# Performance work log

Measured on AMD Instinct MI355X. Metric: run time of the kernel, lower is better.

The kernel has to match this reference:

```python
import jax, jax.numpy as jnp
import numpy as np

IN_FEATURES = 4096
OUT_FEATURES = 4096
DENSE_OUT = int(0.85 * OUT_FEATURES)          # 3481
SPARSE_OUT = OUT_FEATURES - DENSE_OUT         # 615


def setup_inputs() -> dict:
    key = jax.random.key(0)
    kx, kw = jax.random.split(key)
    x = jax.random.normal(kx, (4, 2048, IN_FEATURES), dtype=jnp.float32)
    weights = jax.random.normal(kw, (OUT_FEATURES, IN_FEATURES), dtype=jnp.float32)
    return {"x": x, "weights": weights}


def reference(x, weights):
    # Module partitions weight rows: first SPARSE_OUT rows go through sputnik
    # SpMM, the remaining DENSE_OUT rows through a cutlass GEMM, then outputs
    # are concatenated as [sparse, dense] -> identical to x @ weights.T.
    size_out = x.shape[:-1] + (OUT_FEATURES,)
    xf = x.reshape(-1, x.shape[-1])                      # [N, in]
    w_sparse = weights[:SPARSE_OUT, :]                   # [615, in]
    w_dense = weights[SPARSE_OUT:, :]                    # [3481, in]
    out_sparse = jnp.einsum('ni,oi->no', xf, w_sparse)   # SpMM branch
    out_dense = jnp.einsum('ni,oi->no', xf, w_dense)     # GEMM branch
    out = jnp.concatenate([out_sparse, out_dense], axis=1)
    return out.reshape(size_out)
```

## Files before the change

kernel.cpp:

```cpp
#include <hip/hip_runtime.h>
#include <hip/hip_bf16.h>
#include <cstdint>
#include <cstddef>

#define K_DIM 4096
#define N_DIM 4096
#define BM 128
#define BN 128
#define BK 64

typedef __attribute__((ext_vector_type(8))) short short8;
typedef __attribute__((ext_vector_type(4))) float floatx4;

__device__ __forceinline__ unsigned short f32_bf16_rne(float f) {
    union { float f; unsigned u; } v; v.f = f;
    unsigned r = (v.u + 0x7FFFu + ((v.u >> 16) & 1u)) >> 16;
    return (unsigned short)r;
}

__global__ __launch_bounds__(256) void cast2_f32_bf16_kernel(
        const float* __restrict__ x, const float* __restrict__ w,
        unsigned short* __restrict__ a16, unsigned short* __restrict__ b16,
        long nx, long nw) {
    const long nchunks = (nx + nw) / 8;
    long c = (long)blockIdx.x * 256 + threadIdx.x;
    const long stride = (long)gridDim.x * 256;
    const long xc = nx / 8;
    for (; c < nchunks; c += stride) {
        const float* src;
        unsigned short* dst;
        long i;
        if (c < xc) { i = c * 8;        src = x + i; dst = a16 + i; }
        else        { i = (c - xc) * 8; src = w + i; dst = b16 + i; }
        floatx4 a = *(const floatx4*)(src);
        floatx4 b = *(const floatx4*)(src + 4);
        union { unsigned short u[8]; short8 v; } r;
#pragma unroll
        for (int j = 0; j < 4; j++) r.u[j] = f32_bf16_rne(a[j]);
#pragma unroll
        for (int j = 0; j < 4; j++) r.u[4 + j] = f32_bf16_rne(b[j]);
        *(short8*)(dst) = r.v;
    }
}

__global__ __launch_bounds__(256) void gemm_bf16_bt(
        const unsigned short* __restrict__ A,
        const unsigned short* __restrict__ B,
        float* __restrict__ C, int M) {
    __shared__ unsigned short sA[BM * BK];
    __shared__ unsigned short sB[BN * BK];

    const int tid  = threadIdx.x;
    const int lane = tid & 63;
    const int wave = tid >> 6;
    const int wm   = wave >> 1;
    const int wn   = wave & 1;
    const int quad = lane >> 4;
    const int l16  = lane & 15;

    const int bm = blockIdx.y;
    const int bn = blockIdx.x;

    const int srow     = wave * 8 + (lane >> 3);
    const int kblk_src = (lane & 7) ^ ((lane >> 3) & 7);

    const unsigned short* ag = A + ((size_t)bm * BM + srow) * K_DIM + kblk_src * 8;
    const unsigned short* bg = B + ((size_t)bn * BN + srow) * K_DIM + kblk_src * 8;

    floatx4 acc[4][4];
#pragma unroll
    for (int i = 0; i < 4; i++)
#pragma unroll
        for (int j = 0; j < 4; j++)
            acc[i][j] = (floatx4)0.0f;

    for (int k0 = 0; k0 < K_DIM; k0 += BK) {
#pragma unroll
        for (int i = 0; i < 4; i++) {
            __builtin_amdgcn_global_load_lds(
                (const __attribute__((address_space(1))) void*)(ag + (size_t)(i * 32) * K_DIM),
                (__attribute__((address_space(3))) void*)(sA + (i * 32 + wave * 8) * BK),
                16, 0, 0);
            __builtin_amdgcn_global_load_lds(
                (const __attribute__((address_space(1))) void*)(bg + (size_t)(i * 32) * K_DIM),
                (__attribute__((address_space(3))) void*)(sB + (i * 32 + wave * 8) * BK),
                16, 0, 0);
        }
        ag += BK;
        bg += BK;
        __syncthreads();

#pragma unroll
        for (int s = 0; s < 2; s++) {
            const int pblk = ((s * 4 + quad) ^ (l16 & 7)) * 8;
            short8 af[4], bf[4];
#pragma unroll
            for (int mt = 0; mt < 4; mt++)
                af[mt] = *(const short8*)(sA + (wm * 64 + mt * 16 + l16) * BK + pblk);
#pragma unroll
            for (int nt = 0; nt < 4; nt++)
                bf[nt] = *(const short8*)(sB + (wn * 64 + nt * 16 + l16) * BK + pblk);
#pragma unroll
            for (int mt = 0; mt < 4; mt++)
#pragma unroll
                for (int nt = 0; nt < 4; nt++)
                    acc[mt][nt] = __builtin_amdgcn_mfma_f32_16x16x32_bf16(
                        af[mt], bf[nt], acc[mt][nt], 0, 0, 0);
        }
        __syncthreads();
    }

#pragma unroll
    for (int mt = 0; mt < 4; mt++) {
#pragma unroll
        for (int nt = 0; nt < 4; nt++) {
            const int col = bn * BN + wn * 64 + nt * 16 + l16;
            const size_t row0 = (size_t)bm * BM + wm * 64 + mt * 16 + quad * 4;
#pragma unroll
            for (int r = 0; r < 4; r++)
                C[(row0 + r) * N_DIM + col] = acc[mt][nt][r];
        }
    }
}

__global__ __launch_bounds__(256) void gemm_naive_f32(
        const float* __restrict__ X, const float* __restrict__ W,
        float* __restrict__ C, long total) {
    long idx = (long)blockIdx.x * 256 + threadIdx.x;
    if (idx >= total) return;
    const long row = idx / N_DIM, col = idx % N_DIM;
    const float* x = X + row * K_DIM;
    const float* w = W + col * K_DIM;
    float s = 0.f;
    for (int k = 0; k < K_DIM; k += 4) {
        floatx4 a = *(const floatx4*)(x + k);
        floatx4 b = *(const floatx4*)(w + k);
        s += a[0] * b[0] + a[1] * b[1] + a[2] * b[2] + a[3] * b[3];
    }
    C[idx] = s;
}

extern "C" void kernel_launch(void* const* d_in, const int* in_sizes, int n_in,
                              void* d_out, int out_size, void* d_ws, size_t ws_size,
                              hipStream_t stream) {
    const float* x = (const float*)d_in[0];
    const float* w = (const float*)d_in[1];
    float* out = (float*)d_out;

    const long nx = (long)in_sizes[0];
    const long nw = (long)in_sizes[1];
    const int  M  = (int)(nx / K_DIM);

    const size_t a_bytes = (size_t)nx * 2;
    const size_t b_bytes = (size_t)nw * 2;

    if (ws_size >= a_bytes + b_bytes) {
        unsigned short* a16 = (unsigned short*)d_ws;
        unsigned short* b16 = (unsigned short*)((char*)d_ws + a_bytes);
        cast2_f32_bf16_kernel<<<4096, 256, 0, stream>>>(x, w, a16, b16, nx, nw);
        dim3 grid(N_DIM / BN, M / BM);
        gemm_bf16_bt<<<grid, 256, 0, stream>>>(a16, b16, out, M);
    } else {
        const long total = (long)M * N_DIM;
        gemm_naive_f32<<<(int)((total + 255) / 256), 256, 0, stream>>>(x, w, out, total);
    }
}
```

Baseline: 532.0 us.

## Switch GEMM to 32x32x16 bf16 MFMA and flatten cast kernel grid

The bf16 GEMM inner loop now uses 32x32x16 MFMA instructions on 2x2 tiles per wave instead of 16x16x32 on 4x4 tiles. This halves the LDS fragment loads per k-step and cuts the MFMA instruction count, and the accumulator layout and epilogue indexing change to match. The cast kernel drops its grid-stride loop and launches one thread per 8-element chunk, so many more blocks are launched. The new epilogue writes rows strided by 8, which may change how well stores coalesce.

```diff
diff --git a/kernel.cpp b/kernel.cpp
--- a/kernel.cpp
+++ b/kernel.cpp
@@ -11,6 +11,7 @@
 
 typedef __attribute__((ext_vector_type(8))) short short8;
 typedef __attribute__((ext_vector_type(4))) float floatx4;
+typedef __attribute__((ext_vector_type(16))) float floatx16;
 
 __device__ __forceinline__ unsigned short f32_bf16_rne(float f) {
     union { float f; unsigned u; } v; v.f = f;
@@ -23,24 +24,21 @@
         unsigned short* __restrict__ a16, unsigned short* __restrict__ b16,
         long nx, long nw) {
     const long nchunks = (nx + nw) / 8;
-    long c = (long)blockIdx.x * 256 + threadIdx.x;
-    const long stride = (long)gridDim.x * 256;
+    const long c = (long)blockIdx.x * 256 + threadIdx.x;
+    if (c >= nchunks) return;
     const long xc = nx / 8;
-    for (; c < nchunks; c += stride) {
-        const float* src;
-        unsigned short* dst;
-        long i;
-        if (c < xc) { i = c * 8;        src = x + i; dst = a16 + i; }
-        else        { i = (c - xc) * 8; src = w + i; dst = b16 + i; }
-        floatx4 a = *(const floatx4*)(src);
-        floatx4 b = *(const floatx4*)(src + 4);
-        union { unsigned short u[8]; short8 v; } r;
+    const float* src;
+    unsigned short* dst;
+    if (c < xc) { long i = c * 8;        src = x + i; dst = a16 + i; }
+    else        { long i = (c - xc) * 8; src = w + i; dst = b16 + i; }
+    floatx4 a = *(const floatx4*)(src);
+    floatx4 b = *(const floatx4*)(src + 4);
+    union { unsigned short u[8]; short8 v; } r;
 #pragma unroll
-        for (int j = 0; j < 4; j++) r.u[j] = f32_bf16_rne(a[j]);
+    for (int j = 0; j < 4; j++) r.u[j] = f32_bf16_rne(a[j]);
 #pragma unroll
-        for (int j = 0; j < 4; j++) r.u[4 + j] = f32_bf16_rne(b[j]);
-        *(short8*)(dst) = r.v;
-    }
+    for (int j = 0; j < 4; j++) r.u[4 + j] = f32_bf16_rne(b[j]);
+    *(short8*)(dst) = r.v;
 }
 
 __global__ __launch_bounds__(256) void gemm_bf16_bt(
@@ -55,8 +53,8 @@
     const int wave = tid >> 6;
     const int wm   = wave >> 1;
     const int wn   = wave & 1;
-    const int quad = lane >> 4;
-    const int l16  = lane & 15;
+    const int l32  = lane & 31;
+    const int khalf = lane >> 5;
 
     const int bm = blockIdx.y;
     const int bn = blockIdx.x;
@@ -67,12 +65,12 @@
     const unsigned short* ag = A + ((size_t)bm * BM + srow) * K_DIM + kblk_src * 8;
     const unsigned short* bg = B + ((size_t)bn * BN + srow) * K_DIM + kblk_src * 8;
 
-    floatx4 acc[4][4];
+    floatx16 acc[2][2];
 #pragma unroll
-    for (int i = 0; i < 4; i++)
+    for (int i = 0; i < 2; i++)
 #pragma unroll
-        for (int j = 0; j < 4; j++)
-            acc[i][j] = (floatx4)0.0f;
+        for (int j = 0; j < 2; j++)
+            acc[i][j] = (floatx16)0.0f;
 
     for (int k0 = 0; k0 < K_DIM; k0 += BK) {
 #pragma unroll
@@ -91,34 +89,36 @@
         __syncthreads();
 
 #pragma unroll
-        for (int s = 0; s < 2; s++) {
-            const int pblk = ((s * 4 + quad) ^ (l16 & 7)) * 8;
-            short8 af[4], bf[4];
+        for (int kk = 0; kk < 4; kk++) {
+            const int pblk = ((kk * 2 + khalf) ^ (l32 & 7)) * 8;
+            short8 af[2], bf[2];
 #pragma unroll
-            for (int mt = 0; mt < 4; mt++)
-                af[mt] = *(const short8*)(sA + (wm * 64 + mt * 16 + l16) * BK + pblk);
+            for (int mt = 0; mt < 2; mt++)
+                af[mt] = *(const short8*)(sA + (wm * 64 + mt * 32 + l32) * BK + pblk);
 #pragma unroll
-            for (int nt = 0; nt < 4; nt++)
-                bf[nt] = *(const short8*)(sB + (wn * 64 + nt * 16 + l16) * BK + pblk);
+            for (int nt = 0; nt < 2; nt++)
+                bf[nt] = *(const short8*)(sB + (wn * 64 + nt * 32 + l32) * BK + pblk);
 #pragma unroll
-            for (int mt = 0; mt < 4; mt++)
+            for (int mt = 0; mt < 2; mt++)
 #pragma unroll
-                for (int nt = 0; nt < 4; nt++)
-                    acc[mt][nt] = __builtin_amdgcn_mfma_f32_16x16x32_bf16(
+                for (int nt = 0; nt < 2; nt++)
+                    acc[mt][nt] = __builtin_amdgcn_mfma_f32_32x32x16_bf16(
                         af[mt], bf[nt], acc[mt][nt], 0, 0, 0);
         }
         __syncthreads();
     }
 
 #pragma unroll
-    for (int mt = 0; mt < 4; mt++) {
+    for (int mt = 0; mt < 2; mt++) {
 #pragma unroll
-        for (int nt = 0; nt < 4; nt++) {
-            const int col = bn * BN + wn * 64 + nt * 16 + l16;
-            const size_t row0 = (size_t)bm * BM + wm * 64 + mt * 16 + quad * 4;
+        for (int nt = 0; nt < 2; nt++) {
+            const int col = bn * BN + wn * 64 + nt * 32 + l32;
+            const size_t row0 = (size_t)bm * BM + wm * 64 + mt * 32 + 4 * khalf;
 #pragma unroll
-            for (int r = 0; r < 4; r++)
-                C[(row0 + r) * N_DIM + col] = acc[mt][nt][r];
+            for (int r = 0; r < 16; r++) {
+                const size_t row = row0 + (r & 3) + 8 * (r >> 2);
+                C[row * N_DIM + col] = acc[mt][nt][r];
+            }
         }
     }
 }
@@ -157,7 +157,9 @@
     if (ws_size >= a_bytes + b_bytes) {
         unsigned short* a16 = (unsigned short*)d_ws;
         unsigned short* b16 = (unsigned short*)((char*)d_ws + a_bytes);
-        cast2_f32_bf16_kernel<<<4096, 256, 0, stream>>>(x, w, a16, b16, nx, nw);
+        const long nchunks = (nx + nw) / 8;
+        const int cast_blocks = (int)((nchunks + 255) / 256);
+        cast2_f32_bf16_kernel<<<cast_blocks, 256, 0, stream>>>(x, w, a16, b16, nx, nw);
         dim3 grid(N_DIM / BN, M / BM);
         gemm_bf16_bt<<<grid, 256, 0, stream>>>(a16, b16, out, M);
     } else {
```

Measured after the change: 532.0 us. About the same (+0.0%).
